# Optimization experiments

Hardware: AMD Instinct MI355X
Metric: run time of the kernel (lower is better)

The kernel has to match this reference:

```python
import jax, jax.numpy as jnp
import numpy as np
from jax import lax

T = 5        # unrolled ISTA iterations (module default)
LAM = 0.1    # soft-threshold level (module default)
B, L, K = 4096, 4096, 128


def _conv1d_same(x, k):
    """TF-style SAME cross-correlation. x: [B, L], k: [K] -> [B, L]."""
    Kw = k.shape[0]
    pad_left = (Kw - 1) // 2
    pad_right = Kw - 1 - pad_left
    out = lax.conv_general_dilated(
        x[:, None, :],            # [B, 1, L]
        k[None, None, :],         # [O=1, I=1, K]
        window_strides=(1,),
        padding=[(pad_left, pad_right)],
        dimension_numbers=("NCH", "OIH", "NCH"),
    )
    return out[:, 0, :]


def setup_inputs() -> dict:
    key = jax.random.key(0)
    k1, k2 = jax.random.split(key)
    y = jax.random.normal(k1, (B, L), dtype=jnp.float32)
    thz_pulse = jax.random.normal(k2, (K,), dtype=jnp.float32)  # learned pulse (trainable)
    step_size = jnp.full((1,), 0.1, dtype=jnp.float32)          # learned step (trainable)
    return {"y": y, "thz_pulse": thz_pulse, "step_size": step_size}


def reference(y, thz_pulse, step_size):
    x = jnp.zeros_like(y)
    h = thz_pulse           # matched-filter kernel
    h_rev = thz_pulse[::-1] # time-reversed kernel (adjoint / correlation)
    s = step_size[0]
    for _ in range(T):
        conv_out = _conv1d_same(y, h)           # H y
        residual = y - conv_out                 # y - H y
        update = _conv1d_same(residual, h_rev)  # H^T residual
        x = x + s * update                      # gradient step
        x = jnp.sign(x) * jax.nn.relu(jnp.abs(x) - LAM)  # soft-threshold
    return x
```

## Files before the change

kernel.cpp:

```cpp
#include <hip/hip_runtime.h>


typedef __bf16 bf16;
typedef __bf16 bf16x4 __attribute__((ext_vector_type(4)));
typedef __bf16 bf16x8 __attribute__((ext_vector_type(8)));
typedef float f32x4 __attribute__((ext_vector_type(4)));

#define LC 512
#define PY 808
#define LAM 0.1f

__global__ __launch_bounds__(256, 4) void ista_mfma(
    const float* __restrict__ y, const float* __restrict__ h,
    const float* __restrict__ step, float* __restrict__ out) {
  __shared__ __align__(16) bf16 buf[16 * PY + 64];
  __shared__ float hs[128];

  const int tid = threadIdx.x;
  const int lane = tid & 63;
  const int wave = tid >> 6;
  const int li = lane & 15;
  const int quad = lane >> 4;
  const int chunk0 = blockIdx.x * LC;
  const int b0 = blockIdx.y * 16;

  if (tid < 128) hs[tid] = h[tid];

  {
    const int rr = tid >> 4;
    const int t = tid & 15;
    const float* yrow = y + (size_t)(b0 + rr) * 4096 + (chunk0 - 128);
    bf16* dst = buf + rr * PY;
    if (chunk0 >= 128 && chunk0 + 672 <= 4096) {
      for (int s4 = t; s4 < 200; s4 += 16) {
        float4 v = *reinterpret_cast<const float4*>(yrow + s4 * 4);
        bf16x4 bv;
        bv[0] = (bf16)v.x; bv[1] = (bf16)v.y;
        bv[2] = (bf16)v.z; bv[3] = (bf16)v.w;
        *reinterpret_cast<bf16x4*>(dst + s4 * 4) = bv;
      }
    } else {
      for (int s4 = t; s4 < 200; s4 += 16) {
        int l = chunk0 - 128 + s4 * 4;
        float4 v;
        v.x = (l + 0 >= 0 && l + 0 < 4096) ? yrow[s4 * 4 + 0] : 0.f;
        v.y = (l + 1 >= 0 && l + 1 < 4096) ? yrow[s4 * 4 + 1] : 0.f;
        v.z = (l + 2 >= 0 && l + 2 < 4096) ? yrow[s4 * 4 + 2] : 0.f;
        v.w = (l + 3 >= 0 && l + 3 < 4096) ? yrow[s4 * 4 + 3] : 0.f;
        bf16x4 bv;
        bv[0] = (bf16)v.x; bv[1] = (bf16)v.y;
        bv[2] = (bf16)v.z; bv[3] = (bf16)v.w;
        *reinterpret_cast<bf16x4*>(dst + s4 * 4) = bv;
      }
    }
  }
  __syncthreads();

  bf16x8 A1[5], A2[5];
#pragma unroll
  for (int dd = 0; dd < 5; ++dd) {
    int d = (dd - 2) * 32;
    bf16x8 a1, a2;
#pragma unroll
    for (int j = 0; j < 8; ++j) {
      int k = quad * 8 + j;
      int idx1 = 63 + d + k - li;
      a1[j] = (idx1 >= 0 && idx1 < 128) ? (bf16)hs[idx1] : (bf16)0.f;
      int idx2 = 64 + li - d - k;
      a2[j] = (idx2 >= 0 && idx2 < 128) ? (bf16)(-hs[idx2]) : (bf16)0.f;
    }
    A1[dd] = a1; A2[dd] = a2;
  }

  bf16x4 rv[11];
  const bool edge = (chunk0 == 0) || (chunk0 + LC == 4096);
#pragma unroll
  for (int i = 0; i < 11; ++i) {
    const int t = wave + 4 * i;
    const int i0 = -64 + 16 * t;
    const bf16* base = buf + li * PY + (i0 + 128);
    f32x4 acc;
    {
      bf16x4 yv = *reinterpret_cast<const bf16x4*>(base + quad * 4);
      acc[0] = -(float)yv[0]; acc[1] = -(float)yv[1];
      acc[2] = -(float)yv[2]; acc[3] = -(float)yv[3];
    }
#pragma unroll
    for (int dd = 0; dd < 5; ++dd) {
      bf16x8 bfrag = *reinterpret_cast<const bf16x8*>(
          base + (dd - 2) * 32 + quad * 8);
      acc = __builtin_amdgcn_mfma_f32_16x16x32_bf16(A1[dd], bfrag, acc, 0, 0, 0);
    }
    if (edge) {
#pragma unroll
      for (int e = 0; e < 4; ++e) {
        int g = chunk0 + i0 + quad * 4 + e;
        rv[i][e] = (bf16)((g >= 0 && g < 4096) ? acc[e] : 0.f);
      }
    } else {
#pragma unroll
      for (int e = 0; e < 4; ++e) rv[i][e] = (bf16)acc[e];
    }
  }
  __syncthreads();

#pragma unroll
  for (int i = 0; i < 11; ++i) {
    const int t = wave + 4 * i;
    const int i0 = -64 + 16 * t;
    *reinterpret_cast<bf16x4*>(buf + li * PY + (i0 + 64) + quad * 4) = rv[i];
  }
  __syncthreads();

  const float s = step[0];
#pragma unroll
  for (int i = 0; i < 8; ++i) {
    const int t = wave + 4 * i;
    const int i0 = 16 * t;
    const bf16* base = buf + li * PY + (i0 + 64);
    f32x4 acc = {0.f, 0.f, 0.f, 0.f};
#pragma unroll
    for (int dd = 0; dd < 5; ++dd) {
      bf16x8 bfrag = *reinterpret_cast<const bf16x8*>(
          base + (dd - 2) * 32 + quad * 8);
      acc = __builtin_amdgcn_mfma_f32_16x16x32_bf16(A2[dd], bfrag, acc, 0, 0, 0);
    }
    float4 xv;
#pragma unroll
    for (int e = 0; e < 4; ++e) {
      float su = s * acc[e];
      float ax = fmaxf(fabsf(su) - LAM, 0.f);
      (&xv.x)[e] = copysignf(5.f * ax, su);
    }
    *reinterpret_cast<float4*>(
        out + (size_t)(b0 + li) * 4096 + chunk0 + i0 + quad * 4) = xv;
  }
}

extern "C" void kernel_launch(void* const* d_in, const int* in_sizes, int n_in,
                              void* d_out, int out_size, void* d_ws,
                              size_t ws_size, hipStream_t stream) {
  const float* y = (const float*)d_in[0];
  const float* h = (const float*)d_in[1];
  const float* s = (const float*)d_in[2];
  float* out = (float*)d_out;
  ista_mfma<<<dim3(4096 / LC, 256), dim3(256), 0, stream>>>(y, h, s, out);
}
```

Measured before the change: 150.1 us.

## Collapse two convolutions into one precomputed composite kernel with edge fixup

Folds the two sequential convolutions (H then H^T on the residual) into a single 255-tap kernel (delta-shifted h minus the autocorrelation of h), which a tiny precompute kernel builds into MFMA fragments in workspace. The main kernel then runs one 9-step MFMA convolution per tile directly on y, dropping the intermediate residual pass, its LDS round-trip and two barriers. The composite kernel is only exact away from the sequence boundaries where zero-padding of the residual matters, so a third kernel recomputes the first and last 64 outputs per row in fp32. This adds two extra launches and a separate fixup pass over the row edges.

```diff
diff --git a/kernel.cpp b/kernel.cpp
--- a/kernel.cpp
+++ b/kernel.cpp
@@ -7,14 +7,47 @@
 typedef float f32x4 __attribute__((ext_vector_type(4)));
 
 #define LC 512
-#define PY 808
+#define PY 792
 #define LAM 0.1f
 
-__global__ __launch_bounds__(256, 4) void ista_mfma(
-    const float* __restrict__ y, const float* __restrict__ h,
-    const float* __restrict__ step, float* __restrict__ out) {
-  __shared__ __align__(16) bf16 buf[16 * PY + 64];
-  __shared__ float hs[128];
+__global__ __launch_bounds__(256) void ista_precomp(
+    const float* __restrict__ h, bf16* __restrict__ wfrag) {
+  __shared__ float hl[128];
+  __shared__ float cf[288];
+  const int tid = threadIdx.x;
+  if (tid < 128) hl[tid] = h[tid];
+  cf[tid] = 0.f;
+  if (tid < 32) cf[256 + tid] = 0.f;
+  __syncthreads();
+  {
+    int d = tid - 127;
+    int lag = d - 1;
+    float ac = 0.f;
+    for (int n = 0; n < 128; ++n) {
+      int m = n + lag;
+      float hm = (m >= 0 && m < 128) ? hl[m] : 0.f;
+      ac = fmaf(hl[n], hm, ac);
+    }
+    float cd = ((d >= -63 && d <= 64) ? hl[64 - d] : 0.f) - ac;
+    cf[d + 128] = cd;
+  }
+  __syncthreads();
+  for (int e = tid; e < 9 * 64; e += 256) {
+    int dd = e >> 6, lane = e & 63, li = lane & 15, quad = lane >> 4;
+    bf16x8 f;
+#pragma unroll
+    for (int j = 0; j < 8; ++j) {
+      int d = -128 + dd * 32 + quad * 8 + j - li;
+      f[j] = (bf16)((d >= -128) ? cf[d + 128] : 0.f);
+    }
+    reinterpret_cast<bf16x8*>(wfrag)[e] = f;
+  }
+}
+
+__global__ __launch_bounds__(256, 4) void ista_main(
+    const float* __restrict__ y, const float* __restrict__ step,
+    const bf16* __restrict__ wfrag, float* __restrict__ out) {
+  __shared__ __align__(16) bf16 ys[16 * PY];
 
   const int tid = threadIdx.x;
   const int lane = tid & 63;
@@ -24,15 +57,18 @@
   const int chunk0 = blockIdx.x * LC;
   const int b0 = blockIdx.y * 16;
 
-  if (tid < 128) hs[tid] = h[tid];
+  bf16x8 A[9];
+#pragma unroll
+  for (int dd = 0; dd < 9; ++dd)
+    A[dd] = reinterpret_cast<const bf16x8*>(wfrag)[dd * 64 + lane];
 
   {
     const int rr = tid >> 4;
     const int t = tid & 15;
     const float* yrow = y + (size_t)(b0 + rr) * 4096 + (chunk0 - 128);
-    bf16* dst = buf + rr * PY;
-    if (chunk0 >= 128 && chunk0 + 672 <= 4096) {
-      for (int s4 = t; s4 < 200; s4 += 16) {
+    bf16* dst = ys + rr * PY;
+    if (chunk0 >= 128 && chunk0 + 656 <= 4096) {
+      for (int s4 = t; s4 < 196; s4 += 16) {
         float4 v = *reinterpret_cast<const float4*>(yrow + s4 * 4);
         bf16x4 bv;
         bv[0] = (bf16)v.x; bv[1] = (bf16)v.y;
@@ -40,90 +76,29 @@
         *reinterpret_cast<bf16x4*>(dst + s4 * 4) = bv;
       }
     } else {
-      for (int s4 = t; s4 < 200; s4 += 16) {
+      for (int s4 = t; s4 < 196; s4 += 16) {
         int l = chunk0 - 128 + s4 * 4;
-        float4 v;
-        v.x = (l + 0 >= 0 && l + 0 < 4096) ? yrow[s4 * 4 + 0] : 0.f;
-        v.y = (l + 1 >= 0 && l + 1 < 4096) ? yrow[s4 * 4 + 1] : 0.f;
-        v.z = (l + 2 >= 0 && l + 2 < 4096) ? yrow[s4 * 4 + 2] : 0.f;
-        v.w = (l + 3 >= 0 && l + 3 < 4096) ? yrow[s4 * 4 + 3] : 0.f;
         bf16x4 bv;
-        bv[0] = (bf16)v.x; bv[1] = (bf16)v.y;
-        bv[2] = (bf16)v.z; bv[3] = (bf16)v.w;
+        bv[0] = (bf16)((l + 0 >= 0 && l + 0 < 4096) ? yrow[s4 * 4 + 0] : 0.f);
+        bv[1] = (bf16)((l + 1 >= 0 && l + 1 < 4096) ? yrow[s4 * 4 + 1] : 0.f);
+        bv[2] = (bf16)((l + 2 >= 0 && l + 2 < 4096) ? yrow[s4 * 4 + 2] : 0.f);
+        bv[3] = (bf16)((l + 3 >= 0 && l + 3 < 4096) ? yrow[s4 * 4 + 3] : 0.f);
         *reinterpret_cast<bf16x4*>(dst + s4 * 4) = bv;
       }
     }
   }
   __syncthreads();
 
-  bf16x8 A1[5], A2[5];
-#pragma unroll
-  for (int dd = 0; dd < 5; ++dd) {
-    int d = (dd - 2) * 32;
-    bf16x8 a1, a2;
-#pragma unroll
-    for (int j = 0; j < 8; ++j) {
-      int k = quad * 8 + j;
-      int idx1 = 63 + d + k - li;
-      a1[j] = (idx1 >= 0 && idx1 < 128) ? (bf16)hs[idx1] : (bf16)0.f;
-      int idx2 = 64 + li - d - k;
-      a2[j] = (idx2 >= 0 && idx2 < 128) ? (bf16)(-hs[idx2]) : (bf16)0.f;
-    }
-    A1[dd] = a1; A2[dd] = a2;
-  }
-
-  bf16x4 rv[11];
-  const bool edge = (chunk0 == 0) || (chunk0 + LC == 4096);
-#pragma unroll
-  for (int i = 0; i < 11; ++i) {
-    const int t = wave + 4 * i;
-    const int i0 = -64 + 16 * t;
-    const bf16* base = buf + li * PY + (i0 + 128);
-    f32x4 acc;
-    {
-      bf16x4 yv = *reinterpret_cast<const bf16x4*>(base + quad * 4);
-      acc[0] = -(float)yv[0]; acc[1] = -(float)yv[1];
-      acc[2] = -(float)yv[2]; acc[3] = -(float)yv[3];
-    }
-#pragma unroll
-    for (int dd = 0; dd < 5; ++dd) {
-      bf16x8 bfrag = *reinterpret_cast<const bf16x8*>(
-          base + (dd - 2) * 32 + quad * 8);
-      acc = __builtin_amdgcn_mfma_f32_16x16x32_bf16(A1[dd], bfrag, acc, 0, 0, 0);
-    }
-    if (edge) {
-#pragma unroll
-      for (int e = 0; e < 4; ++e) {
-        int g = chunk0 + i0 + quad * 4 + e;
-        rv[i][e] = (bf16)((g >= 0 && g < 4096) ? acc[e] : 0.f);
-      }
-    } else {
-#pragma unroll
-      for (int e = 0; e < 4; ++e) rv[i][e] = (bf16)acc[e];
-    }
-  }
-  __syncthreads();
-
-#pragma unroll
-  for (int i = 0; i < 11; ++i) {
-    const int t = wave + 4 * i;
-    const int i0 = -64 + 16 * t;
-    *reinterpret_cast<bf16x4*>(buf + li * PY + (i0 + 64) + quad * 4) = rv[i];
-  }
-  __syncthreads();
-
   const float s = step[0];
 #pragma unroll
   for (int i = 0; i < 8; ++i) {
-    const int t = wave + 4 * i;
-    const int i0 = 16 * t;
-    const bf16* base = buf + li * PY + (i0 + 64);
+    const int i0 = 16 * (wave + 4 * i);
+    const bf16* base = ys + li * PY + i0 + quad * 8;
     f32x4 acc = {0.f, 0.f, 0.f, 0.f};
 #pragma unroll
-    for (int dd = 0; dd < 5; ++dd) {
-      bf16x8 bfrag = *reinterpret_cast<const bf16x8*>(
-          base + (dd - 2) * 32 + quad * 8);
-      acc = __builtin_amdgcn_mfma_f32_16x16x32_bf16(A2[dd], bfrag, acc, 0, 0, 0);
+    for (int dd = 0; dd < 9; ++dd) {
+      bf16x8 bfrag = *reinterpret_cast<const bf16x8*>(base + dd * 32);
+      acc = __builtin_amdgcn_mfma_f32_16x16x32_bf16(A[dd], bfrag, acc, 0, 0, 0);
     }
     float4 xv;
 #pragma unroll
@@ -137,6 +112,49 @@
   }
 }
 
+__global__ __launch_bounds__(256) void ista_fixup(
+    const float* __restrict__ y, const float* __restrict__ h,
+    const float* __restrict__ step, float* __restrict__ out) {
+  __shared__ float hl[128];
+  __shared__ float yl[4][192];
+  __shared__ float rl[4][128];
+  const int tid = threadIdx.x;
+  const int lane = tid & 63;
+  const int w = tid >> 6;
+  if (tid < 128) hl[tid] = h[tid];
+  const int g = blockIdx.x * 4 + w;
+  const int row = g >> 1;
+  const int side = g & 1;
+  const float* yr = y + (size_t)row * 4096;
+  const int ybase = side ? 3904 : 0;
+  for (int k = lane; k < 192; k += 64) yl[w][k] = yr[ybase + k];
+  __syncthreads();
+  const int rbase = side ? 3968 : 0;
+#pragma unroll
+  for (int half = 0; half < 2; ++half) {
+    int ip = rbase + lane + 64 * half;
+    float acc = 0.f;
+    for (int j = 0; j < 128; ++j) {
+      int yc = ip + j - 63;
+      float yv = (yc >= 0 && yc < 4096) ? yl[w][yc - ybase] : 0.f;
+      acc = fmaf(hl[j], yv, acc);
+    }
+    rl[w][ip - rbase] = yl[w][ip - ybase] - acc;
+  }
+  __syncthreads();
+  const int i = (side ? 4032 : 0) + lane;
+  float u = 0.f;
+  for (int n = 0; n < 128; ++n) {
+    int ir = i + 64 - n;
+    float rv = (ir >= rbase && ir < rbase + 128 && ir < 4096)
+                   ? rl[w][ir - rbase] : 0.f;
+    u = fmaf(hl[n], rv, u);
+  }
+  float su = step[0] * u;
+  float ax = fmaxf(fabsf(su) - LAM, 0.f);
+  out[(size_t)row * 4096 + i] = copysignf(5.f * ax, su);
+}
+
 extern "C" void kernel_launch(void* const* d_in, const int* in_sizes, int n_in,
                               void* d_out, int out_size, void* d_ws,
                               size_t ws_size, hipStream_t stream) {
@@ -144,5 +162,8 @@
   const float* h = (const float*)d_in[1];
   const float* s = (const float*)d_in[2];
   float* out = (float*)d_out;
-  ista_mfma<<<dim3(4096 / LC, 256), dim3(256), 0, stream>>>(y, h, s, out);
+  bf16* wfrag = (bf16*)d_ws;
+  ista_precomp<<<dim3(1), dim3(256), 0, stream>>>(h, wfrag);
+  ista_main<<<dim3(4096 / LC, 256), dim3(256), 0, stream>>>(y, s, wfrag, out);
+  ista_fixup<<<dim3(4096 * 2 / 4), dim3(256), 0, stream>>>(y, h, s, out);
 }
```

Measured after the change: 187.5 us. +24.9%, slower.
